# Performance work log

Hardware: AMD Instinct MI355X
Metric: run time of the kernel (lower is better)

## Reference

```python
import math
import jax, jax.numpy as jnp
import numpy as np

E = 1024          # emb_size
H = 16            # num_heads
D = E // H        # head_dim
B, S = 4, 2048
DI = 64           # intent dim
K = 32            # num intent clusters
ASSIGN_W = 0.5
MU_W = 0.5
UNC_W = 0.5
EXPLORE_SCALE = 0.5
EXPLOIT_SCALE = 0.5
TEMP_MIN = 0.5
TEMP_MAX = 2.0


def setup_inputs() -> dict:
    key = jax.random.key(0)
    ks = jax.random.split(key, 16)
    inp = {
        "his_emb": jax.random.normal(ks[0], (B, S, E), dtype=jnp.float32),
        "src_key_padding_mask": jax.random.randint(ks[1], (B, S), 0, 2).astype(bool),
        "intent_mu": jax.random.normal(ks[2], (B, S, DI), dtype=jnp.float32),
        "intent_sigma": jax.random.uniform(ks[3], (B, S, DI), dtype=jnp.float32),
        "intent_assign": jax.random.uniform(ks[4], (B, S, K), dtype=jnp.float32),
        "explore": jax.random.uniform(ks[5], (B, S), dtype=jnp.float32),
        "exploit": jax.random.uniform(ks[6], (B, S), dtype=jnp.float32),
    }
    std = 0.02
    inp["Wq"] = jax.random.normal(ks[7], (E, E), dtype=jnp.float32) * std
    inp["bq"] = jnp.zeros((E,), dtype=jnp.float32)
    inp["Wk"] = jax.random.normal(ks[8], (E, E), dtype=jnp.float32) * std
    inp["bk"] = jnp.zeros((E,), dtype=jnp.float32)
    inp["Wv"] = jax.random.normal(ks[9], (E, E), dtype=jnp.float32) * std
    inp["bv"] = jnp.zeros((E,), dtype=jnp.float32)
    inp["Wo"] = jax.random.normal(ks[10], (E, E), dtype=jnp.float32) * std
    inp["bo"] = jnp.zeros((E,), dtype=jnp.float32)
    return inp


def _forward(his_emb, src_key_padding_mask, intent_mu, intent_sigma, intent_assign,
             explore, exploit, Wq, bq, Wk, bk, Wv, bv, Wo, bo):
    b, s, _ = his_emb.shape
    # projections -> [b, h, s, d]
    def proj(W, bias):
        return (his_emb @ W.T + bias).reshape(b, s, H, D).transpose(0, 2, 1, 3)
    q, k, v = proj(Wq, bq), proj(Wk, bk), proj(Wv, bv)

    logits = jnp.einsum("bhqd,bhkd->bhqk", q, k) / math.sqrt(D)  # [b,h,s,s]

    # intent bias [b, s, s]
    assign_sim = jnp.einsum("bqc,bkc->bqk", intent_assign, intent_assign)
    bias = ASSIGN_W * assign_sim
    # mean squared distance via expansion (avoids [b,s,s,DI] intermediate)
    sq = jnp.sum(intent_mu * intent_mu, axis=-1)  # [b,s]
    dot = jnp.einsum("bqd,bkd->bqk", intent_mu, intent_mu)
    mu_dist = (sq[:, :, None] + sq[:, None, :] - 2.0 * dot) / DI
    bias = bias - MU_W * mu_dist
    uncertainty = jnp.mean(intent_sigma, axis=-1)[:, None, :]  # [b,1,s] over keys
    bias = bias - UNC_W * uncertainty

    logits = logits + bias[:, None, :, :]

    attn_mask = src_key_padding_mask[:, None, None, :]  # [b,1,1,s]
    logits = jnp.where(attn_mask, -1e16, logits)

    # per-query temperature scaling
    temperature = 1.0 + EXPLORE_SCALE * explore - EXPLOIT_SCALE * exploit
    temperature = jnp.clip(temperature, TEMP_MIN, TEMP_MAX)
    temperature = jnp.where(src_key_padding_mask, 1.0, temperature)  # [b,s]
    logits = logits / temperature[:, None, :, None]

    probs = jax.nn.softmax(logits, axis=-1)
    probs = jnp.where(attn_mask, 0.0, probs)
    probs = probs / jnp.maximum(jnp.sum(probs, axis=-1, keepdims=True), 1e-8)

    out = jnp.einsum("bhqk,bhkd->bhqd", probs, v)
    out = out.transpose(0, 2, 1, 3).reshape(b, s, E)
    out = out @ Wo.T + bo
    return jnp.where(src_key_padding_mask[:, :, None], 0.0, out)


def reference(his_emb, src_key_padding_mask, intent_mu, intent_sigma, intent_assign,
              explore, exploit, Wq, bq, Wk, bk, Wv, bv, Wo, bo):
    return _forward(his_emb, src_key_padding_mask, intent_mu, intent_sigma,
                    intent_assign, explore, exploit, Wq, bq, Wk, bk, Wv, bv, Wo, bo)
```

## Files before the change

### kernel.cpp

```cpp
#include <hip/hip_runtime.h>
#include <hip/hip_bf16.h>
#include <stdint.h>
#include <stddef.h>

#define Bn 4
#define Sn 2048
#define En 1024
#define Hn 16
#define DIn 64
#define BSn (Bn*Sn)
#define L2E 1.44269504089f
#define SH8L 11.5415603271f

typedef __attribute__((ext_vector_type(8))) short short8;
typedef __attribute__((ext_vector_type(4))) short short4v;
typedef __attribute__((ext_vector_type(4))) float fx4;
typedef __attribute__((ext_vector_type(16))) float fx16;
typedef __attribute__((ext_vector_type(8))) _Float16 half8;
typedef __attribute__((ext_vector_type(2))) __fp16 fp16x2;
typedef __attribute__((ext_vector_type(4))) int ix4;

__device__ __forceinline__ short f2bf(float f){
  union U { __hip_bfloat16 h; short s; } u; u.h = __float2bfloat16(f); return u.s;
}
__device__ __forceinline__ short f2h(float f){
  _Float16 h = (_Float16)f; return __builtin_bit_cast(short, h);
}

__device__ __forceinline__ void async16(const void* g, void* l){
  __builtin_amdgcn_global_load_lds((const __attribute__((address_space(1))) unsigned int*)g,
                                   (__attribute__((address_space(3))) unsigned int*)l, 16, 0, 0);
}

__device__ __forceinline__ fx4 mfma_bf(short8 a, short8 b, fx4 c){
  return __builtin_amdgcn_mfma_f32_16x16x32_bf16(a, b, c, 0, 0, 0);
}
__device__ __forceinline__ fx4 mfma_h(short8 a, short8 b, fx4 c){
  return __builtin_amdgcn_mfma_f32_16x16x32_f16(__builtin_bit_cast(half8, a),
                                                __builtin_bit_cast(half8, b), c, 0, 0, 0);
}
__device__ __forceinline__ fx16 mfma32h(short8 a, short8 b, fx16 c){
  return __builtin_amdgcn_mfma_f32_32x32x16_f16(__builtin_bit_cast(half8, a),
                                                __builtin_bit_cast(half8, b), c, 0, 0, 0);
}

__global__ void scan_mask_k(const int* __restrict__ mask, int* __restrict__ sidx,
                            int* __restrict__ scnt){
  int b = blockIdx.x;
  const int* mb = mask + (size_t)b*Sn;
  __shared__ int wsum[4];
  int tid = threadIdx.x;
  int v[8]; int c = 0;
  #pragma unroll
  for (int j=0;j<8;j++){ v[j] = (mb[tid*8+j] == 0); c += v[j]; }
  int lane = tid&63, wv = tid>>6;
  int pref = c;
  #pragma unroll
  for (int m=1; m<64; m<<=1){ int o = __shfl_up(pref, m, 64); if (lane >= m) pref += o; }
  if (lane==63) wsum[wv] = pref;
  __syncthreads();
  int wbase = 0;
  for (int wprev=0; wprev<wv; wprev++) wbase += wsum[wprev];
  int pos = wbase + pref - c;
  #pragma unroll
  for (int j=0;j<8;j++){ if (v[j]) sidx[(size_t)b*Sn + pos++] = tid*8+j; }
  if (tid==255) scnt[b] = wbase + pref;
}

__global__ void prep_rows_k(const float* __restrict__ mu, const float* __restrict__ sigma,
                            const float* __restrict__ assign, const float* __restrict__ explore,
                            const float* __restrict__ exploit, const int* __restrict__ mask,
                            _Float16* __restrict__ F, _Float16* __restrict__ G,
                            float* __restrict__ a1L){
  int r = blockIdx.x*4 + (threadIdx.x>>6);
  int lane = threadIdx.x & 63;
  float muv = mu[(size_t)r*DIn + lane];
  float sgv = sigma[(size_t)r*DIn + lane];
  float sq = muv*muv, sg = sgv;
  #pragma unroll
  for (int m=32; m; m>>=1){ sq += __shfl_xor(sq,m,64); sg += __shfl_xor(sg,m,64); }
  float unc = sg*(1.f/64.f);
  #pragma unroll
  for (int cb=0; cb<128; cb+=64){
    int col = cb + lane;
    float fv, gv;
    if (col < 32){ float a = assign[(size_t)r*32 + col]; fv = 0.5f*a; gv = a; }
    else if (col < 96){ float m2 = mu[(size_t)r*DIn + (col-32)]; fv = m2*(1.f/64.f); gv = m2; }
    else if (col == 96){ fv = -sq*(1.f/128.f); gv = 1.f; }
    else if (col == 97){ fv = 1.f; gv = -(sq*(1.f/128.f) + 0.5f*unc); }
    else { fv = 0.f; gv = 0.f; }
    F[(size_t)r*128 + col] = (_Float16)fv;
    G[(size_t)r*128 + col] = (_Float16)gv;
  }
  if (lane == 0){
    int mk = mask[r];
    float t = 1.f + 0.5f*explore[r] - 0.5f*exploit[r];
    t = fminf(fmaxf(t, 0.5f), 2.f);
    if (mk) t = 1.f;
    a1L[r] = 0.125f/t * L2E;
  }
}

__global__ __launch_bounds__(256) void gather_x_k(
    const float* __restrict__ his, const int* __restrict__ sidx, const int* __restrict__ scnt,
    const float* __restrict__ a1L, short* __restrict__ Xc, float* __restrict__ a1Lc)
{
  int b = blockIdx.y, jb = blockIdx.x;
  int cnt = scnt[b];
  int scp = (cnt + 127) & ~127;
  int j0 = jb*64;
  if (j0 >= scp) return;
  __shared__ int sj[64];
  int tid = threadIdx.x;
  if (tid < 64){
    int j = j0 + tid;
    int s = (j < cnt) ? sidx[(size_t)b*Sn + j] : -1;
    sj[tid] = s;
    a1Lc[(size_t)b*Sn + j] = (s >= 0) ? a1L[(size_t)b*Sn + s] : 1.0f;
  }
  __syncthreads();
  const float* hb = his + (size_t)b*Sn*En;
  short* Xb_ = Xc + ((size_t)b*Sn + j0)*En;
  #pragma unroll 4
  for (int it=0; it<64; it++){
    int i = it*256 + tid;
    int r = i>>8, c = i&255;
    int s = sj[r];
    short4v o;
    if (s >= 0){
      fx4 v = *(const fx4*)(hb + (size_t)s*En + c*4);
      o = (short4v){ f2bf(v[0]), f2bf(v[1]), f2bf(v[2]), f2bf(v[3]) };
    } else o = (short4v){0,0,0,0};
    *(short4v*)(Xb_ + (size_t)r*En + c*4) = o;
  }
}

__global__ void cast_w_k(const float* __restrict__ Wq, const float* __restrict__ Wk,
                         const float* __restrict__ Wv, const float* __restrict__ Wo,
                         short* __restrict__ WQKV, short* __restrict__ Wof){
  int i = blockIdx.x*256 + threadIdx.x;
  int seg = i >> 18;
  int off = i & 262143;
  const float* src = (seg==0)?Wq:(seg==1)?Wk:(seg==2)?Wv:Wo;
  fx4 v = ((const fx4*)src)[off];
  short4v o;
  if (seg < 3) o = (short4v){ f2bf(v[0]), f2bf(v[1]), f2bf(v[2]), f2bf(v[3]) };
  else         o = (short4v){ f2h(v[0]),  f2h(v[1]),  f2h(v[2]),  f2h(v[3])  };
  if (seg < 3) ((short4v*)WQKV)[(size_t)seg*262144 + off] = o;
  else         ((short4v*)Wof)[off] = o;
}

__global__ void zero_masked_k(const int* __restrict__ mask, float* __restrict__ out){
  int row = blockIdx.x;
  if (!mask[row]) return;
  fx4 z = {0.f,0.f,0.f,0.f};
  ((fx4*)(out + (size_t)row*En))[threadIdx.x] = z;
}

__global__ __launch_bounds__(256) void gemm_qkv_k(
    const short* __restrict__ A, const short* __restrict__ Wqkv,
    short* __restrict__ Q, short* __restrict__ K, short* __restrict__ Vt,
    const float* __restrict__ bq, const float* __restrict__ bk, const float* __restrict__ bv,
    const int* __restrict__ scnt)
{
  __shared__ short sm[17408];
  short* As = sm;
  short* Bs = sm + 8192;
  short* Ct = sm;
  const int tid = threadIdx.x;
  const int wv = tid>>6, lane = tid&63, quad = lane>>4, l16 = lane&15;
  const int m0 = blockIdx.y*128, n0g = blockIdx.x*128;
  const int bb = m0 >> 11, jloc = m0 & 2047;
  const int scp = (scnt[bb] + 127) & ~127;
  if (jloc >= scp) return;
  const int seg = n0g >> 10, nloc = n0g & 1023;
  const int wm = (wv>>1)*64, wn = (wv&1)*64;
  const int srow = tid>>3, pch = tid&7;
  fx4 acc[4][4] = {};
  for (int k0=0; k0<En; k0+=64){
    __syncthreads();
    #pragma unroll
    for (int i=0; i<4; i++){
      int r = i*32 + srow;
      int c = (pch ^ (r&7))*8;
      int ld = (i*256 + tid)*8;
      async16(A    + (size_t)(m0+r)*En  + k0 + c, &As[ld]);
      async16(Wqkv + (size_t)(n0g+r)*En + k0 + c, &Bs[ld]);
    }
    __syncthreads();
    #pragma unroll
    for (int kk=0; kk<2; kk++){
      short8 af[4], bfr[4];
      #pragma unroll
      for (int mi=0; mi<4; mi++){
        int row = wm + mi*16 + l16;
        af[mi] = *(const short8*)&As[row*64 + (((kk*4+quad) ^ (row&7))*8)];
      }
      #pragma unroll
      for (int ni=0; ni<4; ni++){
        int row = wn + ni*16 + l16;
        bfr[ni] = *(const short8*)&Bs[row*64 + (((kk*4+quad) ^ (row&7))*8)];
      }
      #pragma unroll
      for (int mi=0; mi<4; mi++)
        #pragma unroll
        for (int ni=0; ni<4; ni++)
          acc[mi][ni] = mfma_bf(af[mi], bfr[ni], acc[mi][ni]);
    }
  }
  __syncthreads();
  const float* biasv = (seg == 0) ? bq : (seg == 1) ? bk : bv;
  if (seg < 2){
    short* C = seg ? K : Q;
    #pragma unroll
    for (int mi=0; mi<4; mi++)
      #pragma unroll
      for (int ni=0; ni<4; ni++){
        int col = nloc + wn + ni*16 + l16;
        float b0 = biasv[col];
        #pragma unroll
        for (int rg=0; rg<4; rg++){
          int row = m0 + wm + mi*16 + quad*4 + rg;
          C[(size_t)row*En + col] = f2h(acc[mi][ni][rg] + b0);
        }
      }
  } else {
    #pragma unroll
    for (int mi=0; mi<4; mi++)
      #pragma unroll
      for (int ni=0; ni<4; ni++){
        int lcol = wn + ni*16 + l16;
        int lrow = wm + mi*16 + quad*4;
        float b0 = biasv[nloc + lcol];
        short4v pk;
        #pragma unroll
        for (int rg=0; rg<4; rg++) pk[rg] = f2h(acc[mi][ni][rg] + b0);
        *(short4v*)&Ct[lcol*136 + lrow] = pk;
      }
    __syncthreads();
    int sl = (tid&15)*8;
    #pragma unroll
    for (int e8=0; e8<8; e8++){
      int e_l = e8*16 + (tid>>4);
      fx4 val = *(const fx4*)&Ct[e_l*136 + sl];
      int e_g = nloc + e_l;
      size_t dst = ((size_t)(bb*Hn + (e_g>>6))*64 + (e_g&63))*Sn + jloc + sl;
      *(fx4*)&Vt[dst] = val;
    }
  }
}

__global__ __launch_bounds__(256) void gemm_bias_k(
    const short* __restrict__ G, const short* __restrict__ F, _Float16* __restrict__ biasT,
    const float* __restrict__ a1Lc, const int* __restrict__ sidx, const int* __restrict__ scnt)
{
  __shared__ short As[128*128];
  __shared__ short Bs[128*128];
  const int tid = threadIdx.x, b = blockIdx.z;
  const int cnt = scnt[b];
  const int scp64  = (cnt + 63) & ~63;
  const int scp128 = (cnt + 127) & ~127;
  const int m0 = blockIdx.y*128, n0 = blockIdx.x*128;
  if (m0 >= scp64)  return;
  if (n0 >= scp128) return;
  const int wv = tid>>6, lane = tid&63, quad = lane>>4, l16 = lane&15;
  const int wm = (wv>>1)*64, wn = (wv&1)*64;
  const short* Gb = G + (size_t)b*Sn*128;
  const short* Fb = F + (size_t)b*Sn*128;
  const int* sx = sidx + (size_t)b*Sn;
  #pragma unroll
  for (int i=0; i<8; i++){
    int idx = i*256 + tid;
    int r = idx>>4, cl = idx&15, c = cl ^ (r&7);
    int gr = m0 + r;
    int srow = (gr < cnt) ? sx[gr] : 0;
    async16(Gb + (size_t)srow*128 + c*8, &As[idx*8]);
    int qr = n0 + r;
    int qrow = (qr < cnt) ? sx[qr] : 0;
    async16(Fb + (size_t)qrow*128 + c*8, &Bs[idx*8]);
  }
  __syncthreads();
  fx4 acc[4][4] = {};
  #pragma unroll
  for (int k0=0; k0<128; k0+=32){
    short8 af[4], bfr[4];
    #pragma unroll
    for (int mi=0; mi<4; mi++){
      int row = wm + mi*16 + l16, kc = (k0>>3) + quad, pc = kc ^ (row&7);
      af[mi] = *(const short8*)&As[row*128 + pc*8];
    }
    #pragma unroll
    for (int ni=0; ni<4; ni++){
      int row = wn + ni*16 + l16, kc = (k0>>3) + quad, pc = kc ^ (row&7);
      bfr[ni] = *(const short8*)&Bs[row*128 + pc*8];
    }
    #pragma unroll
    for (int mi=0; mi<4; mi++)
      #pragma unroll
      for (int ni=0; ni<4; ni++)
        acc[mi][ni] = mfma_h(af[mi], bfr[ni], acc[mi][ni]);
  }
  _Float16* bQ = biasT + (size_t)b*Sn*Sn;
  #pragma unroll
  for (int mi=0; mi<4; mi++)
    #pragma unroll
    for (int ni=0; ni<4; ni++){
      int col = n0 + wn + ni*16 + l16;
      int rowb = m0 + wm + mi*16 + quad*4;
      float s8 = 8.f * a1Lc[b*Sn + col];
      short4v pk;
      #pragma unroll
      for (int rg=0; rg<4; rg++){
        int s = rowb + rg;
        short hv;
        if (s >= cnt) hv = (short)0xFC00;
        else hv = f2h(acc[mi][ni][rg]*s8 - SH8L);
        pk[rg] = hv;
      }
      *(short4v*)&bQ[((size_t)(rowb>>3)*Sn + col)*8 + (rowb&7)] = pk;
    }
}

__global__ __launch_bounds__(256) void gemm_out_k(
    const short* __restrict__ A, const short* __restrict__ Bm, float* __restrict__ C,
    const float* __restrict__ biasv, const int* __restrict__ sidx, const int* __restrict__ scnt)
{
  __shared__ short As[128*64];
  __shared__ short Bs[128*64];
  const int tid = threadIdx.x;
  const int wv = tid>>6, lane = tid&63, quad = lane>>4, l16 = lane&15;
  const int m0 = blockIdx.y*128, n0 = blockIdx.x*128;
  const int b = m0 >> 11, jloc = m0 & 2047;
  const int cnt = scnt[b];
  const int scp = (cnt + 127) & ~127;
  if (jloc >= scp) return;
  const int* sx = sidx + (size_t)b*Sn;
  const int wm = (wv>>1)*64, wn = (wv&1)*64;
  const int srow = tid>>3, pch = tid&7;
  fx4 acc[4][4] = {};
  for (int k0=0; k0<En; k0+=64){
    __syncthreads();
    #pragma unroll
    for (int i=0; i<4; i++){
      int r = i*32 + srow;
      int c = (pch ^ (r&7))*8;
      int ld = (i*256 + tid)*8;
      async16(A  + (size_t)(m0+r)*En + k0 + c, &As[ld]);
      async16(Bm + (size_t)(n0+r)*En + k0 + c, &Bs[ld]);
    }
    __syncthreads();
    #pragma unroll
    for (int kk=0; kk<2; kk++){
      short8 af[4], bfr[4];
      #pragma unroll
      for (int mi=0; mi<4; mi++){
        int row = wm + mi*16 + l16;
        af[mi] = *(const short8*)&As[row*64 + (((kk*4+quad) ^ (row&7))*8)];
      }
      #pragma unroll
      for (int ni=0; ni<4; ni++){
        int row = wn + ni*16 + l16;
        bfr[ni] = *(const short8*)&Bs[row*64 + (((kk*4+quad) ^ (row&7))*8)];
      }
      #pragma unroll
      for (int mi=0; mi<4; mi++)
        #pragma unroll
        for (int ni=0; ni<4; ni++)
          acc[mi][ni] = mfma_h(af[mi], bfr[ni], acc[mi][ni]);
    }
  }
  #pragma unroll
  for (int mi=0; mi<4; mi++)
    #pragma unroll
    for (int ni=0; ni<4; ni++)
      #pragma unroll
      for (int rg=0; rg<4; rg++){
        int j = jloc + wm + mi*16 + quad*4 + rg;
        if (j < cnt){
          int row = b*Sn + sx[j];
          int col = n0 + wn + ni*16 + l16;
          C[(size_t)row*En + col] = acc[mi][ni][rg] + biasv[col];
        }
      }
}

__global__ __launch_bounds__(256, 4) void flash7_k(
    const short* __restrict__ Qg, const short* __restrict__ Kg, const short* __restrict__ Vtg,
    const _Float16* __restrict__ biasB, const float* __restrict__ a1Lv,
    const int* __restrict__ scnt, short* __restrict__ AO)
{
  __shared__ short smem[2][2][64*64];
  const int tid = threadIdx.x, wv = tid>>6, lane = tid&63;
  const int l32 = lane&31, hi = lane>>5;
  const int q0 = blockIdx.x*128;
  const int b = blockIdx.y >> 4, h = blockIdx.y & 15;
  const int cnt = scnt[b];
  const int NT = ((cnt + 63) & ~63) >> 6;
  const int scp128 = (cnt + 127) & ~127;
  if (q0 >= scp128) return;
  const short* Qb  = Qg  + (size_t)b*Sn*En + h*64;
  const int q = q0 + wv*32 + l32;
  const float a1L = a1Lv[b*Sn + q];

  const int r0 = tid>>3, c0 = (tid&7) ^ (r0&7);
  const int kr0 = (r0 & 51) | ((r0&4)<<1) | ((r0&8)>>1);
  const short* kA = Kg  + (size_t)b*Sn*En + h*64 + (size_t)kr0*En + c0*8;
  const short* vA = Vtg + (size_t)(b*Hn + h)*64*Sn + (size_t)r0*Sn + c0*8;
  const _Float16* bP = biasB + (size_t)b*Sn*Sn + ((size_t)hi*Sn + q)*8;
  const int ld0 = tid*8;

  auto issue = [&](int buf){
    short* base = &smem[buf][0][0];
    async16(kA,             base + ld0);
    async16(kA + 32*En,     base + 2048 + ld0);
    async16(vA,             base + 4096 + ld0);
    async16(vA + 32*Sn,     base + 4096 + 2048 + ld0);
  };
  if (NT > 0){ issue(0); }
  kA += 64*En; vA += 64;

  short8 qf[4];
  #pragma unroll
  for (int c=0; c<4; c++)
    qf[c] = *(const short8*)(Qb + (size_t)q*En + c*16 + hi*8);

  int koff[2][4], voff[2][4];
  #pragma unroll
  for (int t=0; t<2; t++){
    int m = t*32 + l32;
    #pragma unroll
    for (int c=0; c<4; c++)
      koff[t][c] = m*64 + (((c*2 + hi) ^ (m&7))*8);
  }
  #pragma unroll
  for (int ds=0; ds<2; ds++){
    int rv = ds*32 + l32;
    #pragma unroll
    for (int sc=0; sc<4; sc++)
      voff[ds][sc] = 4096 + rv*64 + (((sc*2 + hi) ^ (rv&7))*8);
  }

  fp16x2 one2; one2[0] = (__fp16)1.0f; one2[1] = (__fp16)1.0f;
  fx16 o0 = {}, o1 = {};
  float psum = 0.f;

  for (int T=0; T<NT; T++){
    __syncthreads();
    const short* base = &smem[T&1][0][0];
    if (T < NT-1){ issue((T&1)^1); kA += 64*En; vA += 64; }

    #pragma unroll
    for (int t=0; t<2; t++){
      half8 bch[2];
      #pragma unroll
      for (int c2=0; c2<2; c2++)
        bch[c2] = *(const half8*)(bP + (size_t)(t*4 + c2*2)*Sn*8);
      fx16 sa = {};
      #pragma unroll
      for (int c=0; c<4; c++){
        short8 ka = *(const short8*)(base + koff[t][c]);
        sa = mfma32h(ka, qf[c], sa);
      }
      #pragma unroll
      for (int c2=0; c2<2; c2++){
        fp16x2 pk_[4];
        #pragma unroll
        for (int jj=0; jj<4; jj++){
          float pa = __builtin_amdgcn_exp2f(fmaf(sa[c2*8 + jj*2],     a1L, (float)bch[c2][jj*2]));
          float pb = __builtin_amdgcn_exp2f(fmaf(sa[c2*8 + jj*2 + 1], a1L, (float)bch[c2][jj*2+1]));
          pk_[jj] = __builtin_amdgcn_cvt_pkrtz(pa, pb);
          psum = __builtin_amdgcn_fdot2(pk_[jj], one2, psum, false);
        }
        ix4 fr = { __builtin_bit_cast(int, pk_[0]), __builtin_bit_cast(int, pk_[1]),
                   __builtin_bit_cast(int, pk_[2]), __builtin_bit_cast(int, pk_[3]) };
        short8 pfr = __builtin_bit_cast(short8, fr);
        int sc = t*2 + c2;
        #pragma unroll
        for (int ds=0; ds<2; ds++){
          short8 va = *(const short8*)(base + voff[ds][sc]);
          if (ds == 0) o0 = mfma32h(va, pfr, o0);
          else         o1 = mfma32h(va, pfr, o1);
        }
      }
    }
    bP += (size_t)8*Sn*8;
  }

  psum += __shfl_xor(psum, 32, 64);
  float linv = 1.f/fmaxf(psum, 1e-30f);

  __syncthreads();
  short* stage = &smem[0][0][0] + wv*2304;
  #pragma unroll
  for (int ds=0; ds<2; ds++){
    const fx16& o = ds ? o1 : o0;
    #pragma unroll
    for (int rq=0; rq<4; rq++){
      int d0 = ds*32 + rq*8 + hi*4;
      short4v pk;
      #pragma unroll
      for (int j=0; j<4; j++) pk[j] = f2h(o[rq*4 + j]*linv);
      *(short4v*)&stage[l32*72 + d0] = pk;
    }
  }
  short* AOb = AO + (size_t)b*Sn*En + h*64;
  #pragma unroll
  for (int rnd=0; rnd<4; rnd++){
    int idx = rnd*64 + lane;
    int r = idx>>3, ch = idx&7;
    fx4 val = *(const fx4*)&stage[r*72 + ch*8];
    *(fx4*)(AOb + (size_t)(q0 + wv*32 + r)*En + ch*8) = val;
  }
}

extern "C" void kernel_launch(void* const* d_in, const int* in_sizes, int n_in,
                              void* d_out, int out_size, void* d_ws, size_t ws_size,
                              hipStream_t stream)
{
  const float* his     = (const float*)d_in[0];
  const int*   mask    = (const int*)  d_in[1];
  const float* mu      = (const float*)d_in[2];
  const float* sigma   = (const float*)d_in[3];
  const float* assign  = (const float*)d_in[4];
  const float* explore = (const float*)d_in[5];
  const float* exploit = (const float*)d_in[6];
  const float* Wq = (const float*)d_in[7];  const float* bq = (const float*)d_in[8];
  const float* Wk = (const float*)d_in[9];  const float* bk = (const float*)d_in[10];
  const float* Wv = (const float*)d_in[11]; const float* bv = (const float*)d_in[12];
  const float* Wo = (const float*)d_in[13]; const float* bo = (const float*)d_in[14];

  char* w = (char*)d_ws;
  size_t off = 0;
  auto alloc = [&](size_t bytes){ void* p = w + off; off += (bytes + 255) & ~(size_t)255; return p; };
  short*     Xc    = (short*)alloc((size_t)BSn*En*2);
  short*     WQKV  = (short*)alloc((size_t)3*En*En*2);
  short*     Wof   = (short*)alloc((size_t)En*En*2);
  short*     Qc    = (short*)alloc((size_t)BSn*En*2);
  short*     Kc    = (short*)alloc((size_t)BSn*En*2);
  short*     Vtc   = (short*)alloc((size_t)BSn*En*2);
  short*     AO    = (short*)alloc((size_t)BSn*En*2);
  _Float16*  F     = (_Float16*)alloc((size_t)BSn*128*2);
  _Float16*  G     = (_Float16*)alloc((size_t)BSn*128*2);
  _Float16*  biasT = (_Float16*)alloc((size_t)Bn*Sn*Sn*2);
  float*     a1Lp  = (float*)alloc((size_t)BSn*4);
  float*     a1Lc  = (float*)alloc((size_t)BSn*4);
  int*       sidx  = (int*)alloc((size_t)BSn*4);
  int*       scnt  = (int*)alloc(256);
  (void)ws_size; (void)in_sizes; (void)n_in; (void)out_size;

  scan_mask_k<<<Bn, 256, 0, stream>>>(mask, sidx, scnt);
  prep_rows_k<<<BSn/4, 256, 0, stream>>>(mu, sigma, assign, explore, exploit, mask, F, G, a1Lp);
  cast_w_k<<<4*En*En/4/256, 256, 0, stream>>>(Wq, Wk, Wv, Wo, WQKV, Wof);
  gather_x_k<<<dim3(Sn/64, Bn), 256, 0, stream>>>(his, sidx, scnt, a1Lp, Xc, a1Lc);
  zero_masked_k<<<BSn, 256, 0, stream>>>(mask, (float*)d_out);
  gemm_qkv_k<<<dim3(3*En/128, BSn/128), 256, 0, stream>>>(Xc, WQKV, Qc, Kc, Vtc, bq, bk, bv, scnt);
  gemm_bias_k<<<dim3(Sn/128, Sn/128, Bn), 256, 0, stream>>>(
      (const short*)G, (const short*)F, biasT, a1Lc, sidx, scnt);
  flash7_k<<<dim3(Sn/128, Bn*Hn), 256, 0, stream>>>(Qc, Kc, Vtc, biasT, a1Lc, scnt, AO);
  gemm_out_k<<<dim3(En/128, BSn/128), 256, 0, stream>>>(AO, Wof, (float*)d_out, bo, sidx, scnt);
}
```

Measured before the change: 290.1 us.

## Double-buffer async LDS loads in projection GEMMs and split bias GEMM load

Measured after the change: 281.6 us. 1.03x faster.

```diff
diff --git a/kernel.cpp b/kernel.cpp
--- a/kernel.cpp
+++ b/kernel.cpp
@@ -43,6 +43,12 @@
   return __builtin_amdgcn_mfma_f32_32x32x16_f16(__builtin_bit_cast(half8, a),
                                                 __builtin_bit_cast(half8, b), c, 0, 0, 0);
 }
+
+#define FENCE asm volatile("" ::: "memory")
+#define WAIT_VM4 asm volatile("s_waitcnt vmcnt(4)" ::: "memory")
+#define WAIT_VM8 asm volatile("s_waitcnt vmcnt(8)" ::: "memory")
+#define WAIT_VM0 asm volatile("s_waitcnt vmcnt(0)" ::: "memory")
+#define WAIT_LGKM0 asm volatile("s_waitcnt lgkmcnt(0)" ::: "memory")
 
 __global__ void scan_mask_k(const int* __restrict__ mask, int* __restrict__ sidx,
                             int* __restrict__ scnt){
@@ -164,8 +170,6 @@
     const int* __restrict__ scnt)
 {
   __shared__ short sm[17408];
-  short* As = sm;
-  short* Bs = sm + 8192;
   short* Ct = sm;
   const int tid = threadIdx.x;
   const int wv = tid>>6, lane = tid&63, quad = lane>>4, l16 = lane&15;
@@ -175,38 +179,51 @@
   if (jloc >= scp) return;
   const int seg = n0g >> 10, nloc = n0g & 1023;
   const int wm = (wv>>1)*64, wn = (wv&1)*64;
-  const int srow = tid>>3, pch = tid&7;
+  const int srow = tid>>2, pch = tid&3;
+  auto stage = [&](int kt){
+    int k0 = kt*32;
+    short* dA = sm + ((kt&1)<<12);
+    short* dB = sm + 8192 + ((kt&1)<<12);
+    #pragma unroll
+    for (int i=0; i<2; i++){
+      int r = i*64 + srow;
+      int c = (pch ^ (r&3) ^ ((r>>2)&3))*8;
+      int ld = (i*256 + tid)*8;
+      async16(A    + (size_t)(m0+r)*En  + k0 + c, dA + ld);
+      async16(Wqkv + (size_t)(n0g+r)*En + k0 + c, dB + ld);
+    }
+  };
   fx4 acc[4][4] = {};
-  for (int k0=0; k0<En; k0+=64){
-    __syncthreads();
-    #pragma unroll
-    for (int i=0; i<4; i++){
-      int r = i*32 + srow;
-      int c = (pch ^ (r&7))*8;
-      int ld = (i*256 + tid)*8;
-      async16(A    + (size_t)(m0+r)*En  + k0 + c, &As[ld]);
-      async16(Wqkv + (size_t)(n0g+r)*En + k0 + c, &Bs[ld]);
-    }
-    __syncthreads();
-    #pragma unroll
-    for (int kk=0; kk<2; kk++){
-      short8 af[4], bfr[4];
-      #pragma unroll
-      for (int mi=0; mi<4; mi++){
-        int row = wm + mi*16 + l16;
-        af[mi] = *(const short8*)&As[row*64 + (((kk*4+quad) ^ (row&7))*8)];
-      }
-      #pragma unroll
-      for (int ni=0; ni<4; ni++){
-        int row = wn + ni*16 + l16;
-        bfr[ni] = *(const short8*)&Bs[row*64 + (((kk*4+quad) ^ (row&7))*8)];
-      }
-      #pragma unroll
-      for (int mi=0; mi<4; mi++)
-        #pragma unroll
-        for (int ni=0; ni<4; ni++)
-          acc[mi][ni] = mfma_bf(af[mi], bfr[ni], acc[mi][ni]);
-    }
+  stage(0);
+  #pragma unroll
+  for (int kt=0; kt<32; kt++){
+    if (kt < 31){ stage(kt+1); WAIT_VM4; }
+    else        { WAIT_VM0; }
+    __builtin_amdgcn_s_barrier();
+    FENCE;
+    const short* cA = sm + ((kt&1)<<12);
+    const short* cB = sm + 8192 + ((kt&1)<<12);
+    short8 af[4], bfr[4];
+    #pragma unroll
+    for (int mi=0; mi<4; mi++){
+      int row = wm + mi*16 + l16;
+      int pc = quad ^ (row&3) ^ ((row>>2)&3);
+      af[mi] = *(const short8*)&cA[row*32 + pc*8];
+    }
+    #pragma unroll
+    for (int ni=0; ni<4; ni++){
+      int row = wn + ni*16 + l16;
+      int pc = quad ^ (row&3) ^ ((row>>2)&3);
+      bfr[ni] = *(const short8*)&cB[row*32 + pc*8];
+    }
+    #pragma unroll
+    for (int mi=0; mi<4; mi++)
+      #pragma unroll
+      for (int ni=0; ni<4; ni++)
+        acc[mi][ni] = mfma_bf(af[mi], bfr[ni], acc[mi][ni]);
+    WAIT_LGKM0;
+    __builtin_amdgcn_s_barrier();
+    FENCE;
   }
   __syncthreads();
   const float* biasv = (seg == 0) ? bq : (seg == 1) ? bk : bv;
@@ -254,8 +271,7 @@
     const short* __restrict__ G, const short* __restrict__ F, _Float16* __restrict__ biasT,
     const float* __restrict__ a1Lc, const int* __restrict__ sidx, const int* __restrict__ scnt)
 {
-  __shared__ short As[128*128];
-  __shared__ short Bs[128*128];
+  __shared__ short sm[32768];
   const int tid = threadIdx.x, b = blockIdx.z;
   const int cnt = scnt[b];
   const int scp64  = (cnt + 63) & ~63;
@@ -268,37 +284,50 @@
   const short* Gb = G + (size_t)b*Sn*128;
   const short* Fb = F + (size_t)b*Sn*128;
   const int* sx = sidx + (size_t)b*Sn;
-  #pragma unroll
-  for (int i=0; i<8; i++){
-    int idx = i*256 + tid;
-    int r = idx>>4, cl = idx&15, c = cl ^ (r&7);
-    int gr = m0 + r;
-    int srow = (gr < cnt) ? sx[gr] : 0;
-    async16(Gb + (size_t)srow*128 + c*8, &As[idx*8]);
-    int qr = n0 + r;
-    int qrow = (qr < cnt) ? sx[qr] : 0;
-    async16(Fb + (size_t)qrow*128 + c*8, &Bs[idx*8]);
-  }
-  __syncthreads();
+  int rA[4], rB[4];
+  #pragma unroll
+  for (int i=0; i<4; i++){
+    int s = i*256 + tid;
+    int r = s>>3;
+    int gr = m0 + r;  rA[i] = (gr < cnt) ? sx[gr] : 0;
+    int qr = n0 + r;  rB[i] = (qr < cnt) ? sx[qr] : 0;
+  }
+  #pragma unroll
+  for (int h=0; h<2; h++){
+    #pragma unroll
+    for (int i=0; i<4; i++){
+      int s = i*256 + tid;
+      int r = s>>3, cl8 = s&7;
+      int cg = (h*8 + (cl8 ^ (r&7)))*8;
+      async16(Gb + (size_t)rA[i]*128 + cg, &sm[h*8192 + s*8]);
+      async16(Fb + (size_t)rB[i]*128 + cg, &sm[16384 + h*8192 + s*8]);
+    }
+  }
   fx4 acc[4][4] = {};
   #pragma unroll
-  for (int k0=0; k0<128; k0+=32){
-    short8 af[4], bfr[4];
-    #pragma unroll
-    for (int mi=0; mi<4; mi++){
-      int row = wm + mi*16 + l16, kc = (k0>>3) + quad, pc = kc ^ (row&7);
-      af[mi] = *(const short8*)&As[row*128 + pc*8];
-    }
-    #pragma unroll
-    for (int ni=0; ni<4; ni++){
-      int row = wn + ni*16 + l16, kc = (k0>>3) + quad, pc = kc ^ (row&7);
-      bfr[ni] = *(const short8*)&Bs[row*128 + pc*8];
-    }
-    #pragma unroll
-    for (int mi=0; mi<4; mi++)
-      #pragma unroll
-      for (int ni=0; ni<4; ni++)
-        acc[mi][ni] = mfma_h(af[mi], bfr[ni], acc[mi][ni]);
+  for (int h=0; h<2; h++){
+    if (h == 0){ WAIT_VM8; } else { WAIT_VM0; }
+    __builtin_amdgcn_s_barrier();
+    FENCE;
+    #pragma unroll
+    for (int kk=0; kk<2; kk++){
+      short8 af[4], bfr[4];
+      #pragma unroll
+      for (int mi=0; mi<4; mi++){
+        int row = wm + mi*16 + l16, pc = (kk*4+quad) ^ (row&7);
+        af[mi] = *(const short8*)&sm[h*8192 + row*64 + pc*8];
+      }
+      #pragma unroll
+      for (int ni=0; ni<4; ni++){
+        int row = wn + ni*16 + l16, pc = (kk*4+quad) ^ (row&7);
+        bfr[ni] = *(const short8*)&sm[16384 + h*8192 + row*64 + pc*8];
+      }
+      #pragma unroll
+      for (int mi=0; mi<4; mi++)
+        #pragma unroll
+        for (int ni=0; ni<4; ni++)
+          acc[mi][ni] = mfma_h(af[mi], bfr[ni], acc[mi][ni]);
+    }
   }
   _Float16* bQ = biasT + (size_t)b*Sn*Sn;
   #pragma unroll
@@ -325,8 +354,7 @@
     const short* __restrict__ A, const short* __restrict__ Bm, float* __restrict__ C,
     const float* __restrict__ biasv, const int* __restrict__ sidx, const int* __restrict__ scnt)
 {
-  __shared__ short As[128*64];
-  __shared__ short Bs[128*64];
+  __shared__ short sm[16384];
   const int tid = threadIdx.x;
   const int wv = tid>>6, lane = tid&63, quad = lane>>4, l16 = lane&15;
   const int m0 = blockIdx.y*128, n0 = blockIdx.x*128;
@@ -336,38 +364,51 @@
   if (jloc >= scp) return;
   const int* sx = sidx + (size_t)b*Sn;
   const int wm = (wv>>1)*64, wn = (wv&1)*64;
-  const int srow = tid>>3, pch = tid&7;
+  const int srow = tid>>2, pch = tid&3;
+  auto stage = [&](int kt){
+    int k0 = kt*32;
+    short* dA = sm + ((kt&1)<<12);
+    short* dB = sm + 8192 + ((kt&1)<<12);
+    #pragma unroll
+    for (int i=0; i<2; i++){
+      int r = i*64 + srow;
+      int c = (pch ^ (r&3) ^ ((r>>2)&3))*8;
+      int ld = (i*256 + tid)*8;
+      async16(A  + (size_t)(m0+r)*En + k0 + c, dA + ld);
+      async16(Bm + (size_t)(n0+r)*En + k0 + c, dB + ld);
+    }
+  };
   fx4 acc[4][4] = {};
-  for (int k0=0; k0<En; k0+=64){
-    __syncthreads();
-    #pragma unroll
-    for (int i=0; i<4; i++){
-      int r = i*32 + srow;
-      int c = (pch ^ (r&7))*8;
-      int ld = (i*256 + tid)*8;
-      async16(A  + (size_t)(m0+r)*En + k0 + c, &As[ld]);
-      async16(Bm + (size_t)(n0+r)*En + k0 + c, &Bs[ld]);
-    }
-    __syncthreads();
-    #pragma unroll
-    for (int kk=0; kk<2; kk++){
-      short8 af[4], bfr[4];
-      #pragma unroll
-      for (int mi=0; mi<4; mi++){
-        int row = wm + mi*16 + l16;
-        af[mi] = *(const short8*)&As[row*64 + (((kk*4+quad) ^ (row&7))*8)];
-      }
-      #pragma unroll
-      for (int ni=0; ni<4; ni++){
-        int row = wn + ni*16 + l16;
-        bfr[ni] = *(const short8*)&Bs[row*64 + (((kk*4+quad) ^ (row&7))*8)];
-      }
-      #pragma unroll
-      for (int mi=0; mi<4; mi++)
-        #pragma unroll
-        for (int ni=0; ni<4; ni++)
-          acc[mi][ni] = mfma_h(af[mi], bfr[ni], acc[mi][ni]);
-    }
+  stage(0);
+  #pragma unroll
+  for (int kt=0; kt<32; kt++){
+    if (kt < 31){ stage(kt+1); WAIT_VM4; }
+    else        { WAIT_VM0; }
+    __builtin_amdgcn_s_barrier();
+    FENCE;
+    const short* cA = sm + ((kt&1)<<12);
+    const short* cB = sm + 8192 + ((kt&1)<<12);
+    short8 af[4], bfr[4];
+    #pragma unroll
+    for (int mi=0; mi<4; mi++){
+      int row = wm + mi*16 + l16;
+      int pc = quad ^ (row&3) ^ ((row>>2)&3);
+      af[mi] = *(const short8*)&cA[row*32 + pc*8];
+    }
+    #pragma unroll
+    for (int ni=0; ni<4; ni++){
+      int row = wn + ni*16 + l16;
+      int pc = quad ^ (row&3) ^ ((row>>2)&3);
+      bfr[ni] = *(const short8*)&cB[row*32 + pc*8];
+    }
+    #pragma unroll
+    for (int mi=0; mi<4; mi++)
+      #pragma unroll
+      for (int ni=0; ni<4; ni++)
+        acc[mi][ni] = mfma_h(af[mi], bfr[ni], acc[mi][ni]);
+    WAIT_LGKM0;
+    __builtin_amdgcn_s_barrier();
+    FENCE;
   }
   #pragma unroll
   for (int mi=0; mi<4; mi++)
```
